# Performance work log

Measured on AMD Instinct MI355X. Metric: run time of the kernel, lower is better.

## Reference

```python
import jax, jax.numpy as jnp
import numpy as np

B, L, H = 64, 512, 768

def setup_inputs() -> dict:
    key = jax.random.key(0)
    k1, k2, k3, k4 = jax.random.split(key, 4)
    scale = 1.0 / np.sqrt(H)
    return {
        "hidden_states": jax.random.normal(k1, (B, L, H), dtype=jnp.float32),
        "W_fc": jax.random.normal(k2, (H, H), dtype=jnp.float32) * scale,
        "b_fc": jax.random.normal(k3, (H,), dtype=jnp.float32) * scale,
        "W_nu": jax.random.normal(k4, (H,), dtype=jnp.float32) * scale,
    }

def reference(hidden_states, W_fc, b_fc, W_nu):
    # upsilon = tanh(Linear(hidden_states)); [B, L, H]
    upsilon = jnp.tanh(jnp.einsum("blh,hk->blk", hidden_states, W_fc.T) + b_fc)
    # per-token attention logits: [B, L]  (replaces per-sample torch.mv loop)
    nu = jnp.einsum("blh,h->bl", upsilon, W_nu)
    alphas = jax.nn.softmax(nu, axis=1)
    # weighted-sum pooling: [B, H]  (replaces per-sample torch.mm loop)
    pooled = jnp.einsum("bl,blh->bh", alphas, hidden_states)
    return pooled
```

## Files before the change

kernel.cpp:

```cpp
#include <hip/hip_runtime.h>

#define H_DIM 768
#define B_DIM 64
#define L_DIM 512
#define M_TOT (B_DIM*L_DIM)
#define BM 128
#define BN 128
#define BK 64
#define NB_CNT (H_DIM/BN)
#define KB_CNT (H_DIM/BK)
#define MB_CNT (M_TOT/BM)
#define TILE_HALFS (BM*BK)
#define BUFH 16384

typedef _Float16 f16x8 __attribute__((ext_vector_type(8)));
typedef float f32x4 __attribute__((ext_vector_type(4)));

#define WS_W16   0u
#define WS_NUP   1179648u
#define WS_ALPHA 1966080u
#define WS_POOL  2097152u
#define WS_AIMG  3670016u
#define WS_NEED_IMG (WS_AIMG + (size_t)M_TOT*H_DIM*2)

__device__ __forceinline__ void gload_lds16(const void* g, void* l) {
  __builtin_amdgcn_global_load_lds((const __attribute__((address_space(1))) void*)g,
                                   (__attribute__((address_space(3))) void*)l, 16, 0, 0);
}

__device__ __forceinline__ f16x8 cvt8(const float* src) {
  f32x4 x0 = *(const f32x4*)src;
  f32x4 x1 = *(const f32x4*)(src + 4);
  f16x8 h;
  h[0]=(_Float16)x0[0]; h[1]=(_Float16)x0[1]; h[2]=(_Float16)x0[2]; h[3]=(_Float16)x0[3];
  h[4]=(_Float16)x1[0]; h[5]=(_Float16)x1[1]; h[6]=(_Float16)x1[2]; h[7]=(_Float16)x1[3];
  return h;
}

__device__ __forceinline__ float fast_tanh(float v) {
  float e = __builtin_amdgcn_exp2f(v * 2.8853900817779268f);
  return 1.0f - 2.0f * __builtin_amdgcn_rcpf(e + 1.0f);
}

#define SBAR()  do { __builtin_amdgcn_sched_barrier(0); \
                     __builtin_amdgcn_s_barrier(); \
                     __builtin_amdgcn_sched_barrier(0); } while (0)

__global__ __launch_bounds__(256) void conv_kernel(const float* __restrict__ Wfc,
                                                   const float* __restrict__ hs,
                                                   _Float16* __restrict__ W16,
                                                   _Float16* __restrict__ Aimg) {
  int t = blockIdx.x;
  const float* srcb;
  _Float16* dstb;
  if (t < NB_CNT * KB_CNT) {
    int nb = t / KB_CNT, kb = t % KB_CNT;
    srcb = Wfc + (size_t)(nb*BN)*H_DIM + kb*BK;
    dstb = W16 + (size_t)t*TILE_HALFS;
  } else {
    int u = t - NB_CNT * KB_CNT;
    int mb = u / KB_CNT, kb = u % KB_CNT;
    srcb = hs + (size_t)(mb*BM)*H_DIM + kb*BK;
    dstb = Aimg + (size_t)u*TILE_HALFS;
  }
#pragma unroll
  for (int i = 0; i < 4; ++i) {
    int u = threadIdx.x + i * 256;
    int row = u >> 3, sp = u & 7;
    int sl = sp ^ (row & 7);
    *(f16x8*)(dstb + u*8) = cvt8(srcb + (size_t)row*H_DIM + sl*8);
  }
}

__device__ __forceinline__ void stage128(const _Float16* at, const _Float16* wt,
                                         _Float16* Lb, int tid) {
#pragma unroll
  for (int i = 0; i < 4; ++i) {
    int e = (tid + i*256) * 8;
    gload_lds16(at + e, Lb + e);
  }
#pragma unroll
  for (int i = 0; i < 4; ++i) {
    int e = (tid + i*256) * 8;
    gload_lds16(wt + e, Lb + 8192 + e);
  }
}

__device__ __forceinline__ void rd_frags(const _Float16* base, const int aoff[4],
                                         const int boff[4], int slot,
                                         f16x8 af[4], f16x8 bf[4]) {
#pragma unroll
  for (int mi = 0; mi < 4; ++mi) af[mi] = *(const f16x8*)(base + aoff[mi] + slot);
#pragma unroll
  for (int ni = 0; ni < 4; ++ni) bf[ni] = *(const f16x8*)(base + boff[ni] + slot);
}

__device__ __forceinline__ void mfma16(const f16x8 af[4], const f16x8 bf[4],
                                       f32x4 acc[4][4]) {
  __builtin_amdgcn_s_setprio(1);
#pragma unroll
  for (int mi = 0; mi < 4; ++mi)
#pragma unroll
    for (int ni = 0; ni < 4; ++ni)
      acc[mi][ni] = __builtin_amdgcn_mfma_f32_16x16x32_f16(af[mi], bf[ni], acc[mi][ni], 0, 0, 0);
  __builtin_amdgcn_s_setprio(0);
}

#define PASS_ITER(P, j) do {                                                   \
    _Float16* bufc_ = ((j) & 1) ? b1 : b0;                                     \
    _Float16* bufn_ = ((j) & 1) ? b0 : b1;                                     \
    rd_frags(bufc_, aoff, boff, slot1, af1, bf1);                              \
    mfma16(af0, bf0, acc);                                                     \
    asm volatile("s_waitcnt lgkmcnt(0)" ::: "memory");                         \
    SBAR();                                                                    \
    if ((P) < 2 || (j) < 10) {                                                 \
      const _Float16* aS = abase + (size_t)(((j) < 10) ? (j) + 2 : (j) - 10) * TILE_HALFS; \
      stage128(aS, wS, bufc_, tid);                                            \
      wS += TILE_HALFS;                                                        \
    }                                                                          \
    if ((P) == 2 && (j) == 10) { asm volatile("s_waitcnt vmcnt(0)" ::: "memory"); } \
    else                       { asm volatile("s_waitcnt vmcnt(8)" ::: "memory"); } \
    SBAR();                                                                    \
    rd_frags(bufn_, aoff, boff, slot0, af0, bf0);                              \
    mfma16(af1, bf1, acc);                                                     \
  } while (0)

#define EPI(P) do {                                                            \
    float s16_[4][4];                                                          \
    _Pragma("unroll") for (int mi = 0; mi < 4; ++mi)                           \
    _Pragma("unroll") for (int r = 0; r < 4; ++r) {                            \
      float s_ = 0.f;                                                          \
      _Pragma("unroll") for (int ni = 0; ni < 4; ++ni)                         \
        s_ = fmaf(fast_tanh(acc[mi][ni][r] + bb[P][ni]), wn[P][ni], s_);       \
      s16_[mi][r] = s_;                                                        \
    }                                                                          \
    if (wc == 0) {                                                             \
      _Pragma("unroll") for (int mi = 0; mi < 4; ++mi)                         \
      _Pragma("unroll") for (int r = 0; r < 4; ++r)                            \
        scr[(wr*64 + mi*16 + lk*4 + r)*20 + lrow] = s16_[mi][r];               \
    }                                                                          \
    asm volatile("s_waitcnt lgkmcnt(0)" ::: "memory");                         \
    SBAR();                                                                    \
    float pa_ = 0.f;                                                           \
    if (tid < 128) {                                                           \
      const f32x4* sp_ = (const f32x4*)(scr + tid*20);                         \
      f32x4 q_ = sp_[0] + sp_[1] + sp_[2] + sp_[3];                            \
      pa_ = q_[0] + q_[1] + q_[2] + q_[3];                                     \
    }                                                                          \
    asm volatile("s_waitcnt lgkmcnt(0)" ::: "memory");                         \
    SBAR();                                                                    \
    if (wc == 1) {                                                             \
      _Pragma("unroll") for (int mi = 0; mi < 4; ++mi)                         \
      _Pragma("unroll") for (int r = 0; r < 4; ++r)                            \
        scr[(wr*64 + mi*16 + lk*4 + r)*20 + lrow] = s16_[mi][r];               \
    }                                                                          \
    asm volatile("s_waitcnt lgkmcnt(0)" ::: "memory");                         \
    SBAR();                                                                    \
    if (tid < 128) {                                                           \
      const f32x4* sp_ = (const f32x4*)(scr + tid*20);                         \
      f32x4 q_ = sp_[0] + sp_[1] + sp_[2] + sp_[3];                            \
      nup[(size_t)(nb0 + (P)) * M_TOT + m0 + tid] = pa_ + q_[0]+q_[1]+q_[2]+q_[3]; \
    }                                                                          \
  } while (0)

__global__ __launch_bounds__(256, 2) void gemm_nu_img_kernel(const _Float16* __restrict__ Aimg,
                                                             const _Float16* __restrict__ W16,
                                                             const float* __restrict__ bfc,
                                                             const float* __restrict__ wnu,
                                                             float* __restrict__ nup) {
  __shared__ __align__(16) _Float16 LS[2 * BUFH];
  __shared__ __align__(16) float scr[128 * 20];

  int bid = blockIdx.x;
  int mb = bid & (MB_CNT - 1);
  int nb0 = (bid >> 8) * 3;
  int m0 = mb * BM;
  int tid = threadIdx.x;
  int wv = tid >> 6, ln = tid & 63;
  int wr = wv >> 1, wc = wv & 1;
  int lrow = ln & 15, lk = ln >> 4;

  f32x4 acc[4][4] = {};
  f16x8 af0[4], bf0[4], af1[4], bf1[4];
  const _Float16* abase = Aimg + (size_t)(mb * KB_CNT) * TILE_HALFS;
  const _Float16* wbase = W16  + (size_t)(nb0 * KB_CNT) * TILE_HALFS;
  _Float16* b0 = LS;
  _Float16* b1 = LS + BUFH;

  int aoff[4], boff[4];
#pragma unroll
  for (int mi = 0; mi < 4; ++mi) aoff[mi] = (wr*64 + mi*16 + lrow) * 64;
#pragma unroll
  for (int ni = 0; ni < 4; ++ni) boff[ni] = 8192 + (wc*64 + ni*16 + lrow) * 64;
  int slot0 = ((0*4 + lk) ^ (lrow & 7)) * 8;
  int slot1 = ((1*4 + lk) ^ (lrow & 7)) * 8;

  float wn[3][4], bb[3][4];
#pragma unroll
  for (int p = 0; p < 3; ++p)
#pragma unroll
    for (int ni = 0; ni < 4; ++ni) {
      int c = (nb0 + p)*BN + wc*64 + ni*16 + lrow;
      wn[p][ni] = wnu[c];
      bb[p][ni] = bfc[c];
    }
  asm volatile("s_waitcnt vmcnt(0)" ::: "memory");

  stage128(abase,              wbase,              b0, tid);
  stage128(abase + TILE_HALFS, wbase + TILE_HALFS, b1, tid);
  const _Float16* wS = wbase + 2 * TILE_HALFS;
  asm volatile("s_waitcnt vmcnt(8)" ::: "memory");
  SBAR();
  rd_frags(b0, aoff, boff, slot0, af0, bf0);

#pragma unroll 1
  for (int j = 0; j < 12; ++j) PASS_ITER(0, j);
  EPI(0);
#pragma unroll
  for (int mi = 0; mi < 4; ++mi)
#pragma unroll
    for (int ni = 0; ni < 4; ++ni) acc[mi][ni] = f32x4{0.f, 0.f, 0.f, 0.f};

#pragma unroll 1
  for (int j = 0; j < 12; ++j) PASS_ITER(1, j);
  EPI(1);
#pragma unroll
  for (int mi = 0; mi < 4; ++mi)
#pragma unroll
    for (int ni = 0; ni < 4; ++ni) acc[mi][ni] = f32x4{0.f, 0.f, 0.f, 0.f};

#pragma unroll 1
  for (int j = 0; j < 11; ++j) PASS_ITER(2, j);
  rd_frags(b1, aoff, boff, slot1, af1, bf1);
  mfma16(af0, bf0, acc);
  mfma16(af1, bf1, acc);
  EPI(2);
}

__global__ __launch_bounds__(256) void gemm_nu_kernel(const float* __restrict__ A,
                                                      const _Float16* __restrict__ W16,
                                                      const float* __restrict__ bfc,
                                                      const float* __restrict__ wnu,
                                                      float* __restrict__ nup) {
  __shared__ __align__(16) _Float16 lsA[TILE_HALFS];
  __shared__ __align__(16) _Float16 lsB[TILE_HALFS];
  __shared__ float nred[2][BM];

  int bid = blockIdx.x;
  int nb = bid % NB_CNT;
  int mb = bid / NB_CNT;
  int m0 = mb * BM, n0 = nb * BN;
  int tid = threadIdx.x;
  int wv = tid >> 6, ln = tid & 63;
  int wr = wv >> 1, wc = wv & 1;
  int lrow = ln & 15, lk = ln >> 4;

  f32x4 acc[4][4] = {};
  const _Float16* wbase = W16 + (size_t)(nb * KB_CNT) * TILE_HALFS;

  for (int kb = 0; kb < KB_CNT; ++kb) {
    const _Float16* wt = wbase + (size_t)kb * TILE_HALFS;
    for (int i = 0; i < 4; ++i) {
      int e = (tid + i*256) * 8;
      gload_lds16(wt + e, lsB + e);
    }
    for (int i = 0; i < 4; ++i) {
      int u = tid + i * 256;
      int row = u >> 3, sl = u & 7;
      *(f16x8*)(lsA + row*BK + ((sl ^ (row & 7)) * 8)) =
          cvt8(A + (size_t)(m0 + row) * H_DIM + kb*BK + sl*8);
    }
    __syncthreads();
#pragma unroll
    for (int kk = 0; kk < 2; ++kk) {
      f16x8 af[4], bf[4];
      int s = kk*4 + lk;
#pragma unroll
      for (int mi = 0; mi < 4; ++mi) {
        int r = wr*64 + mi*16 + lrow;
        af[mi] = *(const f16x8*)(lsA + r*BK + ((s ^ (r & 7)) * 8));
      }
#pragma unroll
      for (int ni = 0; ni < 4; ++ni) {
        int r = wc*64 + ni*16 + lrow;
        bf[ni] = *(const f16x8*)(lsB + r*BK + ((s ^ (r & 7)) * 8));
      }
#pragma unroll
      for (int mi = 0; mi < 4; ++mi)
#pragma unroll
        for (int ni = 0; ni < 4; ++ni)
          acc[mi][ni] = __builtin_amdgcn_mfma_f32_16x16x32_f16(af[mi], bf[ni], acc[mi][ni], 0, 0, 0);
    }
    __syncthreads();
  }

  float wn[4], bb[4];
  for (int ni = 0; ni < 4; ++ni) {
    int c = n0 + wc*64 + ni*16 + lrow;
    wn[ni] = wnu[c];
    bb[ni] = bfc[c];
  }
  for (int mi = 0; mi < 4; ++mi) {
    for (int r = 0; r < 4; ++r) {
      float s = 0.f;
      for (int ni = 0; ni < 4; ++ni)
        s = fmaf(fast_tanh(acc[mi][ni][r] + bb[ni]), wn[ni], s);
      for (int o = 1; o < 16; o <<= 1) s += __shfl_xor(s, o, 64);
      if (lrow == 0) nred[wc][wr*64 + mi*16 + lk*4 + r] = s;
    }
  }
  __syncthreads();
  if (tid < BM)
    nup[(size_t)nb * M_TOT + m0 + tid] = nred[0][tid] + nred[1][tid];
}

__global__ __launch_bounds__(512) void softmax_kernel(const float* __restrict__ nup,
                                                      float* __restrict__ alphas) {
  int b = blockIdx.x;
  int l = threadIdx.x;
  int m = b * L_DIM + l;
  float v = 0.f;
  for (int nb = 0; nb < NB_CNT; ++nb) v += nup[(size_t)nb * M_TOT + m];
  __shared__ float smax[8], ssum[8];
  int w = l >> 6, ln = l & 63;
  float mx = v;
  for (int o = 1; o < 64; o <<= 1) mx = fmaxf(mx, __shfl_xor(mx, o, 64));
  if (ln == 0) smax[w] = mx;
  __syncthreads();
  mx = smax[0];
  for (int i = 1; i < 8; ++i) mx = fmaxf(mx, smax[i]);
  float e = __expf(v - mx);
  float sm = e;
  for (int o = 1; o < 64; o <<= 1) sm += __shfl_xor(sm, o, 64);
  if (ln == 0) ssum[w] = sm;
  __syncthreads();
  float tot = 0.f;
  for (int i = 0; i < 8; ++i) tot += ssum[i];
  alphas[m] = e / tot;
}

__global__ __launch_bounds__(192) void pool1_img_kernel(const _Float16* __restrict__ img,
                                                        const float* __restrict__ alphas,
                                                        float* __restrict__ part) {
  int b = blockIdx.x >> 3;
  int lc = blockIdx.x & 7;
  int tid = threadIdx.x;
  int g = tid % 96, rp = tid / 96;
  int kb = g >> 3, sl = g & 7;
  __shared__ float al[64];
  __shared__ float tmp[2][H_DIM];
  if (tid < 64) al[tid] = alphas[b * L_DIM + lc*64 + tid];
  __syncthreads();
  float s[8] = {};
  for (int l = rp; l < 64; l += 2) {
    int m = b * L_DIM + lc*64 + l;
    int mb = m >> 7, row = m & 127;
    const f16x8* src = (const f16x8*)(img + ((size_t)(mb*KB_CNT + kb))*TILE_HALFS
                                      + row*64 + ((sl ^ (row & 7)) * 8));
    f16x8 h = *src;
    float a = al[l];
#pragma unroll
    for (int j = 0; j < 8; ++j) s[j] = fmaf(a, (float)h[j], s[j]);
  }
#pragma unroll
  for (int j = 0; j < 8; ++j) tmp[rp][g*8 + j] = s[j];
  __syncthreads();
  float* dst = part + ((size_t)lc * B_DIM + b) * H_DIM + tid*4;
  f32x4 o;
#pragma unroll
  for (int q = 0; q < 4; ++q) o[q] = tmp[0][tid*4 + q] + tmp[1][tid*4 + q];
  *(f32x4*)dst = o;
}

__global__ __launch_bounds__(256) void pool1_kernel(const float* __restrict__ hs,
                                                    const float* __restrict__ alphas,
                                                    float* __restrict__ part) {
  int b = blockIdx.x >> 3;
  int lc = blockIdx.x & 7;
  int tid = threadIdx.x;
  __shared__ float al[64];
  if (tid < 64) al[tid] = alphas[b * L_DIM + lc*64 + tid];
  __syncthreads();
  const float* xp = hs + ((size_t)b * L_DIM + lc*64) * H_DIM;
  int h0 = tid * 3;
  float s0 = 0.f, s1 = 0.f, s2 = 0.f;
  for (int l = 0; l < 64; ++l) {
    float a = al[l];
    const float* r = xp + (size_t)l * H_DIM + h0;
    s0 += a * r[0]; s1 += a * r[1]; s2 += a * r[2];
  }
  float* dst = part + ((size_t)lc * B_DIM + b) * H_DIM + h0;
  dst[0] = s0; dst[1] = s1; dst[2] = s2;
}

__global__ __launch_bounds__(256) void pool2_kernel(const float* __restrict__ part,
                                                    float* __restrict__ out) {
  int i = blockIdx.x * 256 + threadIdx.x;
  float s = 0.f;
  for (int lc = 0; lc < 8; ++lc) s += part[(size_t)lc * (B_DIM * H_DIM) + i];
  out[i] = s;
}

extern "C" void kernel_launch(void* const* d_in, const int* in_sizes, int n_in,
                              void* d_out, int out_size, void* d_ws, size_t ws_size,
                              hipStream_t stream) {
  const float* hs  = (const float*)d_in[0];
  const float* Wfc = (const float*)d_in[1];
  const float* bfc = (const float*)d_in[2];
  const float* wnu = (const float*)d_in[3];
  float* out = (float*)d_out;
  char* ws = (char*)d_ws;
  _Float16* W16 = (_Float16*)(ws + WS_W16);
  float* nup    = (float*)(ws + WS_NUP);
  float* alphas = (float*)(ws + WS_ALPHA);
  float* part   = (float*)(ws + WS_POOL);

  bool img = (ws_size >= WS_NEED_IMG);
  _Float16* Aimg = (_Float16*)(ws + WS_AIMG);
  if (img) {
    conv_kernel<<<(NB_CNT + MB_CNT) * KB_CNT, 256, 0, stream>>>(Wfc, hs, W16, Aimg);
    gemm_nu_img_kernel<<<MB_CNT * 2, 256, 0, stream>>>(Aimg, W16, bfc, wnu, nup);
  } else {
    conv_kernel<<<NB_CNT * KB_CNT, 256, 0, stream>>>(Wfc, hs, W16, Aimg);
    gemm_nu_kernel<<<MB_CNT * NB_CNT, 256, 0, stream>>>(hs, W16, bfc, wnu, nup);
  }
  softmax_kernel<<<B_DIM, 512, 0, stream>>>(nup, alphas);
  if (img) {
    pool1_img_kernel<<<B_DIM * 8, 192, 0, stream>>>(Aimg, alphas, part);
  } else {
    pool1_kernel<<<B_DIM * 8, 256, 0, stream>>>(hs, alphas, part);
  }
  pool2_kernel<<<192, 256, 0, stream>>>(part, out);
}
```

Measured before the change: 91.83 us.

## Fuse fp32-to-fp16 activation conversion into the first GEMM pass

The separate conversion of hidden_states is removed. The GEMM now loads fp32 activations in its first N-pass, converts them in registers, and writes them both to LDS and to the global fp16 image. Later passes reuse that image. This drops a full conversion kernel and its extra round trip through memory. In exchange, the first pass is less pipelined, and both N-group blocks redundantly write the same image tiles.

```diff
diff --git a/kernel.cpp b/kernel.cpp
--- a/kernel.cpp
+++ b/kernel.cpp
@@ -37,6 +37,13 @@
   return h;
 }
 
+__device__ __forceinline__ f16x8 cvt8v(f32x4 x0, f32x4 x1) {
+  f16x8 h;
+  h[0]=(_Float16)x0[0]; h[1]=(_Float16)x0[1]; h[2]=(_Float16)x0[2]; h[3]=(_Float16)x0[3];
+  h[4]=(_Float16)x1[0]; h[5]=(_Float16)x1[1]; h[6]=(_Float16)x1[2]; h[7]=(_Float16)x1[3];
+  return h;
+}
+
 __device__ __forceinline__ float fast_tanh(float v) {
   float e = __builtin_amdgcn_exp2f(v * 2.8853900817779268f);
   return 1.0f - 2.0f * __builtin_amdgcn_rcpf(e + 1.0f);
@@ -46,29 +53,17 @@
                      __builtin_amdgcn_s_barrier(); \
                      __builtin_amdgcn_sched_barrier(0); } while (0)
 
-__global__ __launch_bounds__(256) void conv_kernel(const float* __restrict__ Wfc,
-                                                   const float* __restrict__ hs,
-                                                   _Float16* __restrict__ W16,
-                                                   _Float16* __restrict__ Aimg) {
+__global__ __launch_bounds__(256) void wconv_kernel(const float* __restrict__ Wfc,
+                                                    _Float16* __restrict__ W16) {
   int t = blockIdx.x;
-  const float* srcb;
-  _Float16* dstb;
-  if (t < NB_CNT * KB_CNT) {
-    int nb = t / KB_CNT, kb = t % KB_CNT;
-    srcb = Wfc + (size_t)(nb*BN)*H_DIM + kb*BK;
-    dstb = W16 + (size_t)t*TILE_HALFS;
-  } else {
-    int u = t - NB_CNT * KB_CNT;
-    int mb = u / KB_CNT, kb = u % KB_CNT;
-    srcb = hs + (size_t)(mb*BM)*H_DIM + kb*BK;
-    dstb = Aimg + (size_t)u*TILE_HALFS;
-  }
+  int nb = t / KB_CNT, kb = t % KB_CNT;
 #pragma unroll
   for (int i = 0; i < 4; ++i) {
     int u = threadIdx.x + i * 256;
     int row = u >> 3, sp = u & 7;
     int sl = sp ^ (row & 7);
-    *(f16x8*)(dstb + u*8) = cvt8(srcb + (size_t)row*H_DIM + sl*8);
+    *(f16x8*)(W16 + (size_t)t*TILE_HALFS + u*8) =
+        cvt8(Wfc + (size_t)(nb*BN + row)*H_DIM + kb*BK + sl*8);
   }
 }
 
@@ -163,11 +158,12 @@
     }                                                                          \
   } while (0)
 
-__global__ __launch_bounds__(256, 2) void gemm_nu_img_kernel(const _Float16* __restrict__ Aimg,
-                                                             const _Float16* __restrict__ W16,
-                                                             const float* __restrict__ bfc,
-                                                             const float* __restrict__ wnu,
-                                                             float* __restrict__ nup) {
+__global__ __launch_bounds__(256, 2) void gemm_fused_kernel(const float* __restrict__ hs,
+                                                            const _Float16* __restrict__ W16,
+                                                            const float* __restrict__ bfc,
+                                                            const float* __restrict__ wnu,
+                                                            _Float16* __restrict__ Aimg,
+                                                            float* __restrict__ nup) {
   __shared__ __align__(16) _Float16 LS[2 * BUFH];
   __shared__ __align__(16) float scr[128 * 20];
 
@@ -182,8 +178,9 @@
 
   f32x4 acc[4][4] = {};
   f16x8 af0[4], bf0[4], af1[4], bf1[4];
-  const _Float16* abase = Aimg + (size_t)(mb * KB_CNT) * TILE_HALFS;
-  const _Float16* wbase = W16  + (size_t)(nb0 * KB_CNT) * TILE_HALFS;
+  _Float16* imgb = Aimg + (size_t)(mb * KB_CNT) * TILE_HALFS;
+  const _Float16* abase = imgb;
+  const _Float16* wb0 = W16 + (size_t)(nb0 * KB_CNT) * TILE_HALFS;
   _Float16* b0 = LS;
   _Float16* b1 = LS + BUFH;
 
@@ -206,20 +203,74 @@
     }
   asm volatile("s_waitcnt vmcnt(0)" ::: "memory");
 
-  stage128(abase,              wbase,              b0, tid);
-  stage128(abase + TILE_HALFS, wbase + TILE_HALFS, b1, tid);
-  const _Float16* wS = wbase + 2 * TILE_HALFS;
+  {
+    int r0 = tid >> 3, sp = tid & 7;
+    int sl = sp ^ (r0 & 7);
+    const float* asrc = hs + (size_t)(m0 + r0) * H_DIM + sl * 8;
+    f32x4 R[8]; f16x8 H[4];
+#pragma unroll
+    for (int i = 0; i < 4; ++i) {
+      int e = (tid + i*256) * 8;
+      gload_lds16(wb0 + e, b0 + 8192 + e);
+    }
+#pragma unroll
+    for (int i = 0; i < 4; ++i) {
+      const float* p = asrc + (size_t)(32*i) * H_DIM;
+      R[2*i] = *(const f32x4*)p; R[2*i+1] = *(const f32x4*)(p + 4);
+    }
+#pragma unroll
+    for (int i = 0; i < 4; ++i) H[i] = cvt8v(R[2*i], R[2*i+1]);
+
+#pragma unroll 1
+    for (int kb = 0; kb < 12; ++kb) {
+      _Float16* bufc = (kb & 1) ? b1 : b0;
+      _Float16* bufn = (kb & 1) ? b0 : b1;
+      _Float16* idst = imgb + (size_t)kb * TILE_HALFS;
+#pragma unroll
+      for (int i = 0; i < 4; ++i) {
+        int e = (tid + i*256) * 8;
+        *(f16x8*)(bufc + e) = H[i];
+        *(f16x8*)(idst + e) = H[i];
+      }
+      if (kb < 11) {
+#pragma unroll
+        for (int i = 0; i < 4; ++i) {
+          int e = (tid + i*256) * 8;
+          gload_lds16(wb0 + (size_t)(kb+1)*TILE_HALFS + e, bufn + 8192 + e);
+        }
+        const float* an = asrc + (size_t)(kb+1) * BK;
+#pragma unroll
+        for (int i = 0; i < 4; ++i) {
+          const float* p = an + (size_t)(32*i) * H_DIM;
+          R[2*i] = *(const f32x4*)p; R[2*i+1] = *(const f32x4*)(p + 4);
+        }
+      }
+      asm volatile("s_waitcnt lgkmcnt(0)" ::: "memory");
+      SBAR();
+      rd_frags(bufc, aoff, boff, slot0, af0, bf0);
+      mfma16(af0, bf0, acc);
+      rd_frags(bufc, aoff, boff, slot1, af1, bf1);
+      mfma16(af1, bf1, acc);
+      if (kb < 11) {
+#pragma unroll
+        for (int i = 0; i < 4; ++i) H[i] = cvt8v(R[2*i], R[2*i+1]);
+      }
+      SBAR();
+    }
+  }
+
+  const _Float16* w1b = W16 + (size_t)((nb0 + 1) * KB_CNT) * TILE_HALFS;
+  stage128(abase,              w1b,              b0, tid);
+  stage128(abase + TILE_HALFS, w1b + TILE_HALFS, b1, tid);
+  const _Float16* wS = w1b + 2 * TILE_HALFS;
+  EPI(0);
+#pragma unroll
+  for (int mi = 0; mi < 4; ++mi)
+#pragma unroll
+    for (int ni = 0; ni < 4; ++ni) acc[mi][ni] = f32x4{0.f, 0.f, 0.f, 0.f};
   asm volatile("s_waitcnt vmcnt(8)" ::: "memory");
   SBAR();
   rd_frags(b0, aoff, boff, slot0, af0, bf0);
-
-#pragma unroll 1
-  for (int j = 0; j < 12; ++j) PASS_ITER(0, j);
-  EPI(0);
-#pragma unroll
-  for (int mi = 0; mi < 4; ++mi)
-#pragma unroll
-    for (int ni = 0; ni < 4; ++ni) acc[mi][ni] = f32x4{0.f, 0.f, 0.f, 0.f};
 
 #pragma unroll 1
   for (int j = 0; j < 12; ++j) PASS_ITER(1, j);
@@ -417,11 +468,10 @@
 
   bool img = (ws_size >= WS_NEED_IMG);
   _Float16* Aimg = (_Float16*)(ws + WS_AIMG);
+  wconv_kernel<<<NB_CNT * KB_CNT, 256, 0, stream>>>(Wfc, W16);
   if (img) {
-    conv_kernel<<<(NB_CNT + MB_CNT) * KB_CNT, 256, 0, stream>>>(Wfc, hs, W16, Aimg);
-    gemm_nu_img_kernel<<<MB_CNT * 2, 256, 0, stream>>>(Aimg, W16, bfc, wnu, nup);
+    gemm_fused_kernel<<<MB_CNT * 2, 256, 0, stream>>>(hs, W16, bfc, wnu, Aimg, nup);
   } else {
-    conv_kernel<<<NB_CNT * KB_CNT, 256, 0, stream>>>(Wfc, hs, W16, Aimg);
     gemm_nu_kernel<<<MB_CNT * NB_CNT, 256, 0, stream>>>(hs, W16, bfc, wnu, nup);
   }
   softmax_kernel<<<B_DIM, 512, 0, stream>>>(nup, alphas);
```

After: 89.28 us. 2.8% less time.

## Retile GEMM to 256-row blocks with BK=32 tiles and 512 threads

Applied to the files above, without the earlier changes.

Changes the fp16 pre-converted activation and weight images to 32-wide K tiles, with A tiles of 256 rows and a matching swizzle. The fused GEMM+tanh+nu kernel now runs 512 threads (8 waves) over 256 rows per block, so each staged W tile is reused across twice as many rows. The pipeline is restructured so the MFMA on the current fragments runs while the next stage loads. Block index mapping groups 8 M-blocks per N-group for L2 locality. This cuts W traffic and LDS footprint per row, at the cost of twice as many barriers per K and a risk of lower occupancy with 512-thread blocks.

```diff
diff --git a/kernel.cpp b/kernel.cpp
--- a/kernel.cpp
+++ b/kernel.cpp
@@ -11,7 +11,12 @@
 #define KB_CNT (H_DIM/BK)
 #define MB_CNT (M_TOT/BM)
 #define TILE_HALFS (BM*BK)
-#define BUFH 16384
+
+#define KB32 24
+#define MB256 128
+#define AT_H 8192
+#define WT_H 4096
+#define BUF_H 12288
 
 typedef _Float16 f16x8 __attribute__((ext_vector_type(8)));
 typedef float f32x4 __attribute__((ext_vector_type(4)));
@@ -46,53 +51,49 @@
                      __builtin_amdgcn_s_barrier(); \
                      __builtin_amdgcn_sched_barrier(0); } while (0)
 
-__global__ __launch_bounds__(256) void conv_kernel(const float* __restrict__ Wfc,
-                                                   const float* __restrict__ hs,
-                                                   _Float16* __restrict__ W16,
-                                                   _Float16* __restrict__ Aimg) {
+__global__ __launch_bounds__(256) void wconv32_kernel(const float* __restrict__ Wfc,
+                                                      _Float16* __restrict__ W16) {
   int t = blockIdx.x;
-  const float* srcb;
-  _Float16* dstb;
-  if (t < NB_CNT * KB_CNT) {
-    int nb = t / KB_CNT, kb = t % KB_CNT;
-    srcb = Wfc + (size_t)(nb*BN)*H_DIM + kb*BK;
-    dstb = W16 + (size_t)t*TILE_HALFS;
-  } else {
-    int u = t - NB_CNT * KB_CNT;
-    int mb = u / KB_CNT, kb = u % KB_CNT;
-    srcb = hs + (size_t)(mb*BM)*H_DIM + kb*BK;
-    dstb = Aimg + (size_t)u*TILE_HALFS;
-  }
+  int nb = t / KB32, kb = t % KB32;
+  _Float16* dst = W16 + (size_t)t * WT_H;
+#pragma unroll
+  for (int i = 0; i < 2; ++i) {
+    int c = threadIdx.x + i * 256;
+    int row = c >> 2, sp = c & 3;
+    int sl = sp ^ ((row >> 1) & 3);
+    *(f16x8*)(dst + c*8) =
+        cvt8(Wfc + (size_t)(nb*BN + row)*H_DIM + kb*32 + sl*8);
+  }
+}
+
+__global__ __launch_bounds__(256) void aconv32_kernel(const float* __restrict__ A,
+                                                      _Float16* __restrict__ img) {
+  int t = blockIdx.x;
+  int mb = t / KB32, kb = t % KB32;
+  _Float16* dst = img + (size_t)t * AT_H;
 #pragma unroll
   for (int i = 0; i < 4; ++i) {
-    int u = threadIdx.x + i * 256;
-    int row = u >> 3, sp = u & 7;
-    int sl = sp ^ (row & 7);
-    *(f16x8*)(dstb + u*8) = cvt8(srcb + (size_t)row*H_DIM + sl*8);
-  }
-}
-
-__device__ __forceinline__ void stage128(const _Float16* at, const _Float16* wt,
-                                         _Float16* Lb, int tid) {
-#pragma unroll
-  for (int i = 0; i < 4; ++i) {
-    int e = (tid + i*256) * 8;
-    gload_lds16(at + e, Lb + e);
-  }
-#pragma unroll
-  for (int i = 0; i < 4; ++i) {
-    int e = (tid + i*256) * 8;
-    gload_lds16(wt + e, Lb + 8192 + e);
-  }
+    int c = threadIdx.x + i * 256;
+    int row = c >> 2, sp = c & 3;
+    int sl = sp ^ ((row >> 1) & 3);
+    *(f16x8*)(dst + c*8) =
+        cvt8(A + (size_t)(mb*256 + row)*H_DIM + kb*32 + sl*8);
+  }
+}
+
+__device__ __forceinline__ void stage3(const _Float16* aT, const _Float16* wT,
+                                       _Float16* buf, int tid) {
+  gload_lds16(aT + tid*8,         buf + tid*8);
+  gload_lds16(aT + (tid+512)*8,   buf + (tid+512)*8);
+  gload_lds16(wT + tid*8,         buf + 8192 + tid*8);
 }
 
 __device__ __forceinline__ void rd_frags(const _Float16* base, const int aoff[4],
-                                         const int boff[4], int slot,
-                                         f16x8 af[4], f16x8 bf[4]) {
-#pragma unroll
-  for (int mi = 0; mi < 4; ++mi) af[mi] = *(const f16x8*)(base + aoff[mi] + slot);
-#pragma unroll
-  for (int ni = 0; ni < 4; ++ni) bf[ni] = *(const f16x8*)(base + boff[ni] + slot);
+                                         const int boff[4], f16x8 af[4], f16x8 bf[4]) {
+#pragma unroll
+  for (int mi = 0; mi < 4; ++mi) af[mi] = *(const f16x8*)(base + aoff[mi]);
+#pragma unroll
+  for (int ni = 0; ni < 4; ++ni) bf[ni] = *(const f16x8*)(base + boff[ni]);
 }
 
 __device__ __forceinline__ void mfma16(const f16x8 af[4], const f16x8 bf[4],
@@ -106,23 +107,21 @@
   __builtin_amdgcn_s_setprio(0);
 }
 
-#define PASS_ITER(P, j) do {                                                   \
+#define PITER(P, j, FIN, FOUT) do {                                            \
     _Float16* bufc_ = ((j) & 1) ? b1 : b0;                                     \
     _Float16* bufn_ = ((j) & 1) ? b0 : b1;                                     \
-    rd_frags(bufc_, aoff, boff, slot1, af1, bf1);                              \
-    mfma16(af0, bf0, acc);                                                     \
     asm volatile("s_waitcnt lgkmcnt(0)" ::: "memory");                         \
-    SBAR();                                                                    \
-    if ((P) < 2 || (j) < 10) {                                                 \
-      const _Float16* aS = abase + (size_t)(((j) < 10) ? (j) + 2 : (j) - 10) * TILE_HALFS; \
-      stage128(aS, wS, bufc_, tid);                                            \
-      wS += TILE_HALFS;                                                        \
-    }                                                                          \
-    if ((P) == 2 && (j) == 10) { asm volatile("s_waitcnt vmcnt(0)" ::: "memory"); } \
-    else                       { asm volatile("s_waitcnt vmcnt(8)" ::: "memory"); } \
-    SBAR();                                                                    \
-    rd_frags(bufn_, aoff, boff, slot0, af0, bf0);                              \
-    mfma16(af1, bf1, acc);                                                     \
+    SBAR();                                           \
+    if ((P) < 2 || (j) < 22) {                                                 \
+      int j2_ = ((j) < 22) ? (j) + 2 : (j) - 22;                               \
+      stage3(abase + (size_t)j2_ * AT_H, wS, bufc_, tid);                      \
+      wS += WT_H;                                                              \
+    }                                                                          \
+    mfma16(af##FIN, bf##FIN, acc);                                             \
+    if ((P) == 2 && (j) == 22) { asm volatile("s_waitcnt vmcnt(0)" ::: "memory"); } \
+    else                       { asm volatile("s_waitcnt vmcnt(3)" ::: "memory"); } \
+    SBAR();                                             \
+    rd_frags(bufn_, aoff, boff, af##FOUT, bf##FOUT);                           \
   } while (0)
 
 #define EPI(P) do {                                                            \
@@ -142,7 +141,7 @@
     asm volatile("s_waitcnt lgkmcnt(0)" ::: "memory");                         \
     SBAR();                                                                    \
     float pa_ = 0.f;                                                           \
-    if (tid < 128) {                                                           \
+    if (tid < 256) {                                                           \
       const f32x4* sp_ = (const f32x4*)(scr + tid*20);                         \
       f32x4 q_ = sp_[0] + sp_[1] + sp_[2] + sp_[3];                            \
       pa_ = q_[0] + q_[1] + q_[2] + q_[3];                                     \
@@ -156,25 +155,26 @@
     }                                                                          \
     asm volatile("s_waitcnt lgkmcnt(0)" ::: "memory");                         \
     SBAR();                                                                    \
-    if (tid < 128) {                                                           \
+    if (tid < 256) {                                                           \
       const f32x4* sp_ = (const f32x4*)(scr + tid*20);                         \
       f32x4 q_ = sp_[0] + sp_[1] + sp_[2] + sp_[3];                            \
       nup[(size_t)(nb0 + (P)) * M_TOT + m0 + tid] = pa_ + q_[0]+q_[1]+q_[2]+q_[3]; \
     }                                                                          \
   } while (0)
 
-__global__ __launch_bounds__(256, 2) void gemm_nu_img_kernel(const _Float16* __restrict__ Aimg,
+__global__ __launch_bounds__(512, 2) void gemm_nu_img_kernel(const _Float16* __restrict__ Aimg,
                                                              const _Float16* __restrict__ W16,
                                                              const float* __restrict__ bfc,
                                                              const float* __restrict__ wnu,
                                                              float* __restrict__ nup) {
-  __shared__ __align__(16) _Float16 LS[2 * BUFH];
-  __shared__ __align__(16) float scr[128 * 20];
+  __shared__ __align__(16) _Float16 LS[2 * BUF_H];
+  __shared__ __align__(16) float scr[256 * 20];
 
   int bid = blockIdx.x;
-  int mb = bid & (MB_CNT - 1);
-  int nb0 = (bid >> 8) * 3;
-  int m0 = mb * BM;
+  int x = bid & 7, g = (bid >> 3) & 1, c = bid >> 4;
+  int mb = c*8 + x;
+  int nb0 = g * 3;
+  int m0 = mb * 256;
   int tid = threadIdx.x;
   int wv = tid >> 6, ln = tid & 63;
   int wr = wv >> 1, wc = wv & 1;
@@ -182,39 +182,41 @@
 
   f32x4 acc[4][4] = {};
   f16x8 af0[4], bf0[4], af1[4], bf1[4];
-  const _Float16* abase = Aimg + (size_t)(mb * KB_CNT) * TILE_HALFS;
-  const _Float16* wbase = W16  + (size_t)(nb0 * KB_CNT) * TILE_HALFS;
+  const _Float16* abase = Aimg + (size_t)(mb * KB32) * AT_H;
+  const _Float16* wbase = W16  + (size_t)(nb0 * KB32) * WT_H;
   _Float16* b0 = LS;
-  _Float16* b1 = LS + BUFH;
-
+  _Float16* b1 = LS + BUF_H;
+
+  int slot = (lk ^ ((lrow >> 1) & 3)) * 8;
   int aoff[4], boff[4];
 #pragma unroll
-  for (int mi = 0; mi < 4; ++mi) aoff[mi] = (wr*64 + mi*16 + lrow) * 64;
-#pragma unroll
-  for (int ni = 0; ni < 4; ++ni) boff[ni] = 8192 + (wc*64 + ni*16 + lrow) * 64;
-  int slot0 = ((0*4 + lk) ^ (lrow & 7)) * 8;
-  int slot1 = ((1*4 + lk) ^ (lrow & 7)) * 8;
+  for (int mi = 0; mi < 4; ++mi) aoff[mi] = (wr*64 + mi*16 + lrow) * 32 + slot;
+#pragma unroll
+  for (int ni = 0; ni < 4; ++ni) boff[ni] = 8192 + (wc*64 + ni*16 + lrow) * 32 + slot;
 
   float wn[3][4], bb[3][4];
 #pragma unroll
-  for (int p = 0; p < 3; ++p)
+  for (int p = 0; p < 3; ++p) {
 #pragma unroll
     for (int ni = 0; ni < 4; ++ni) {
-      int c = (nb0 + p)*BN + wc*64 + ni*16 + lrow;
-      wn[p][ni] = wnu[c];
-      bb[p][ni] = bfc[c];
+      int cc = (nb0 + p)*BN + wc*64 + ni*16 + lrow;
+      wn[p][ni] = wnu[cc];
+      bb[p][ni] = bfc[cc];
     }
+    asm volatile("" :: "v"(wn[p][0]), "v"(wn[p][1]), "v"(wn[p][2]), "v"(wn[p][3]),
+                       "v"(bb[p][0]), "v"(bb[p][1]), "v"(bb[p][2]), "v"(bb[p][3]));
+  }
   asm volatile("s_waitcnt vmcnt(0)" ::: "memory");
 
-  stage128(abase,              wbase,              b0, tid);
-  stage128(abase + TILE_HALFS, wbase + TILE_HALFS, b1, tid);
-  const _Float16* wS = wbase + 2 * TILE_HALFS;
-  asm volatile("s_waitcnt vmcnt(8)" ::: "memory");
+  stage3(abase,        wbase,        b0, tid);
+  stage3(abase + AT_H, wbase + WT_H, b1, tid);
+  const _Float16* wS = wbase + 2 * WT_H;
+  asm volatile("s_waitcnt vmcnt(3)" ::: "memory");
   SBAR();
-  rd_frags(b0, aoff, boff, slot0, af0, bf0);
+  rd_frags(b0, aoff, boff, af0, bf0);
 
 #pragma unroll 1
-  for (int j = 0; j < 12; ++j) PASS_ITER(0, j);
+  for (int jj = 0; jj < 12; ++jj) { PITER(0, 2*jj, 0, 1); PITER(0, 2*jj+1, 1, 0); }
   EPI(0);
 #pragma unroll
   for (int mi = 0; mi < 4; ++mi)
@@ -222,7 +224,7 @@
     for (int ni = 0; ni < 4; ++ni) acc[mi][ni] = f32x4{0.f, 0.f, 0.f, 0.f};
 
 #pragma unroll 1
-  for (int j = 0; j < 12; ++j) PASS_ITER(1, j);
+  for (int jj = 0; jj < 12; ++jj) { PITER(1, 2*jj, 0, 1); PITER(1, 2*jj+1, 1, 0); }
   EPI(1);
 #pragma unroll
   for (int mi = 0; mi < 4; ++mi)
@@ -230,11 +232,24 @@
     for (int ni = 0; ni < 4; ++ni) acc[mi][ni] = f32x4{0.f, 0.f, 0.f, 0.f};
 
 #pragma unroll 1
-  for (int j = 0; j < 11; ++j) PASS_ITER(2, j);
-  rd_frags(b1, aoff, boff, slot1, af1, bf1);
-  mfma16(af0, bf0, acc);
+  for (int jj = 0; jj < 11; ++jj) { PITER(2, 2*jj, 0, 1); PITER(2, 2*jj+1, 1, 0); }
+  PITER(2, 22, 0, 1);
   mfma16(af1, bf1, acc);
   EPI(2);
+}
+
+__global__ __launch_bounds__(256) void wconv_old_kernel(const float* __restrict__ Wfc,
+                                                        _Float16* __restrict__ W16) {
+  int t = blockIdx.x;
+  int nb = t / KB_CNT, kb = t % KB_CNT;
+#pragma unroll
+  for (int i = 0; i < 4; ++i) {
+    int u = threadIdx.x + i * 256;
+    int row = u >> 3, sp = u & 7;
+    int sl = sp ^ (row & 7);
+    *(f16x8*)(W16 + (size_t)t*TILE_HALFS + u*8) =
+        cvt8(Wfc + (size_t)(nb*BN + row)*H_DIM + kb*BK + sl*8);
+  }
 }
 
 __global__ __launch_bounds__(256) void gemm_nu_kernel(const float* __restrict__ A,
@@ -296,9 +311,9 @@
 
   float wn[4], bb[4];
   for (int ni = 0; ni < 4; ++ni) {
-    int c = n0 + wc*64 + ni*16 + lrow;
-    wn[ni] = wnu[c];
-    bb[ni] = bfc[c];
+    int cc = n0 + wc*64 + ni*16 + lrow;
+    wn[ni] = wnu[cc];
+    bb[ni] = bfc[cc];
   }
   for (int mi = 0; mi < 4; ++mi) {
     for (int r = 0; r < 4; ++r) {
@@ -346,7 +361,7 @@
   int lc = blockIdx.x & 7;
   int tid = threadIdx.x;
   int g = tid % 96, rp = tid / 96;
-  int kb = g >> 3, sl = g & 7;
+  int kb = g >> 2, sl = g & 3;
   __shared__ float al[64];
   __shared__ float tmp[2][H_DIM];
   if (tid < 64) al[tid] = alphas[b * L_DIM + lc*64 + tid];
@@ -354,9 +369,9 @@
   float s[8] = {};
   for (int l = rp; l < 64; l += 2) {
     int m = b * L_DIM + lc*64 + l;
-    int mb = m >> 7, row = m & 127;
-    const f16x8* src = (const f16x8*)(img + ((size_t)(mb*KB_CNT + kb))*TILE_HALFS
-                                      + row*64 + ((sl ^ (row & 7)) * 8));
+    int mb = m >> 8, row = m & 255;
+    const f16x8* src = (const f16x8*)(img + ((size_t)(mb*KB32 + kb))*AT_H
+                                      + row*32 + ((sl ^ ((row >> 1) & 3)) * 8));
     f16x8 h = *src;
     float a = al[l];
 #pragma unroll
@@ -418,10 +433,11 @@
   bool img = (ws_size >= WS_NEED_IMG);
   _Float16* Aimg = (_Float16*)(ws + WS_AIMG);
   if (img) {
-    conv_kernel<<<(NB_CNT + MB_CNT) * KB_CNT, 256, 0, stream>>>(Wfc, hs, W16, Aimg);
-    gemm_nu_img_kernel<<<MB_CNT * 2, 256, 0, stream>>>(Aimg, W16, bfc, wnu, nup);
+    wconv32_kernel<<<NB_CNT * KB32, 256, 0, stream>>>(Wfc, W16);
+    aconv32_kernel<<<MB256 * KB32, 256, 0, stream>>>(hs, Aimg);
+    gemm_nu_img_kernel<<<MB256 * 2, 512, 0, stream>>>(Aimg, W16, bfc, wnu, nup);
   } else {
-    conv_kernel<<<NB_CNT * KB_CNT, 256, 0, stream>>>(Wfc, hs, W16, Aimg);
+    wconv_old_kernel<<<NB_CNT * KB_CNT, 256, 0, stream>>>(Wfc, W16);
     gemm_nu_kernel<<<MB_CNT * NB_CNT, 256, 0, stream>>>(hs, W16, bfc, wnu, nup);
   }
   softmax_kernel<<<B_DIM, 512, 0, stream>>>(nup, alphas);
```

After: 97.72 us. 1.06x slower.
